# Performance work log

Measured on AMD Instinct MI355X. Metric: run time of the kernel, lower is better.

Reference implementation:

```python
import jax, jax.numpy as jnp
import numpy as np

DELTA_VAR = 0.5
DELTA_DIST = 1.5
ALPHA, BETA, GAMMA = 1.0, 1.0, 0.001
EPS = 1e-8


def _safe_sqrt(x):
    # sqrt with zero (sub)gradient at 0, matching torch.norm's subgradient
    pos = x > 0
    return jnp.sqrt(jnp.where(pos, x, 1.0)) * pos


def setup_inputs() -> dict:
    key = jax.random.key(0)
    k1, k2, k3 = jax.random.split(key, 3)
    B, F, H, W, K = 8, 16, 384, 384, 24
    x = jax.random.normal(k1, (B, F, H, W), dtype=jnp.float32)
    n_clusters = jax.random.randint(k2, (B,), 2, K + 1).astype(jnp.int32)
    # per-pixel instance labels, in-range per sample
    labels = jax.random.randint(k3, (B, H * W), 0, K) % n_clusters[:, None]
    target = jax.nn.one_hot(labels, K, dtype=jnp.float32)  # (B, L, K)
    target = target.transpose(0, 2, 1).reshape(B, K, H, W)
    return {"input": x, "target": target, "n_clusters": n_clusters}


def reference(input, target, n_clusters):
    B, F, H, W = input.shape
    K = target.shape[1]
    x = input.reshape(B, F, H * W)          # (b, f, l)
    t = target.reshape(B, K, H * W)         # (b, c, l)
    nc = n_clusters.astype(x.dtype)         # (b,)
    valid = (jnp.arange(K)[None, :] < n_clusters[:, None]).astype(x.dtype)  # (b, c)

    # ---- cluster means (masked segment mean; padded clusters -> 0) ----
    t_sum = t.sum(-1)                                        # (b, c)
    sums = jnp.einsum('bfl,bcl->bfc', x, t)                  # (b, f, c)
    means = sums / (t_sum[:, None, :] + EPS) * valid[:, None, :]

    # ---- variance term: ||x_l - mu_c||_2 via quadratic expansion ----
    x2 = jnp.sum(x * x, axis=1)                              # (b, l)
    m2 = jnp.sum(means * means, axis=1)                      # (b, c)
    xm = jnp.einsum('bfl,bfc->bcl', x, means)                # (b, c, l)
    d2 = jnp.maximum(x2[:, None, :] - 2.0 * xm + m2[:, :, None], 0.0)
    dist = _safe_sqrt(d2)                                    # (b, c, l)
    var = jnp.maximum(dist - DELTA_VAR, 0.0) ** 2 * t        # (b, c, l)
    c_var = var.sum(-1) / (t_sum + EPS)                      # (b, c)
    var_per = (c_var * valid).sum(-1) / (nc + EPS)
    var_term = jnp.sum(var_per * (nc > 0)) / B

    # ---- distance term: hinge on pairwise mean distances ----
    mm = jnp.einsum('bfc,bfd->bcd', means, means)            # (b, c, c)
    pd2 = jnp.maximum(m2[:, :, None] - 2.0 * mm + m2[:, None, :], 0.0)
    pdist = _safe_sqrt(pd2)                                  # (b, c, c)
    offdiag = 1.0 - jnp.eye(K, dtype=x.dtype)
    pair_mask = valid[:, :, None] * valid[:, None, :] * offdiag
    hinge = jnp.maximum(2.0 * DELTA_DIST - pdist, 0.0) ** 2 * pair_mask
    dist_per = hinge.sum((1, 2)) / (2.0 * nc * (nc - 1.0) + EPS)
    dist_term = jnp.sum(dist_per * (nc > 1)) / B

    # ---- regularization term: mean over valid clusters of ||mu_c|| ----
    norms = _safe_sqrt(m2)                                   # (b, c)
    reg_term = jnp.sum((norms * valid).sum(-1) / nc) / B

    return ALPHA * var_term + BETA * dist_term + GAMMA * reg_term
```

## Files before the change

### kernel.cpp

```cpp
#include <hip/hip_runtime.h>

#define B 8
#define F 16
#define K 24
#define L 147456
#define NSEG (L / 256)
#define NBLKB 288
#define KB_ITER 4
#define EPSF 1e-8f
#define DELTA_VAR 0.5f
#define DELTA_DIST 1.5f
#define GAMMA 0.001f

typedef float fx4 __attribute__((ext_vector_type(4)));
typedef short bf16x8 __attribute__((ext_vector_type(8)));
typedef float f32x4 __attribute__((ext_vector_type(4)));

#define OFF_CNTP 3538944
#define OFF_VARP 3981312
#define OFF_CNT  4423680
#define OFF_VSUM 4424448
#define OFF_MEAN 4425216
#define OFF_LAB  4437504

__device__ __forceinline__ short to_bf16(float v) {
    unsigned u = __float_as_uint(v);
    return (short)((u + 0x7FFFu + ((u >> 16) & 1u)) >> 16);
}

__global__ __launch_bounds__(256) void ka_labels(const float* __restrict__ t,
                                                 unsigned char* __restrict__ labels,
                                                 float* __restrict__ cnt_part) {
    const int blk = blockIdx.x;
    const int b = blk / NSEG;
    const int seg = blk % NSEG;
    const int tid = threadIdx.x;
    const int l = seg * 256 + tid;

    int lab = 0;
    #pragma unroll
    for (int c = 0; c < K; ++c) {
        float tv = __builtin_nontemporal_load(&t[(size_t)(b * K + c) * L + l]);
        lab += c * (tv > 0.5f);
    }
    labels[(size_t)b * L + l] = (unsigned char)lab;

    __shared__ float cnt[32];
    if (tid < 32) cnt[tid] = 0.f;
    __syncthreads();
    atomicAdd(&cnt[lab], 1.f);
    __syncthreads();
    if (tid < K) cnt_part[blk * K + tid] = cnt[tid];
}

__global__ __launch_bounds__(256) void kr_reduce24(const float* __restrict__ part,
                                                   float* __restrict__ out) {
    const int bc = blockIdx.x;
    const int b = bc / K;
    const int c = bc % K;
    const int tid = threadIdx.x;
    float s = 0.f;
    for (int j = tid; j < NSEG; j += 256) s += part[(b * NSEG + j) * K + c];
    __shared__ float red[256];
    red[tid] = s;
    __syncthreads();
    for (int st = 128; st > 0; st >>= 1) {
        if (tid < st) red[tid] += red[tid + st];
        __syncthreads();
    }
    if (tid == 0) out[bc] = red[0];
}

__global__ __launch_bounds__(256) void kb_mfma(const float* __restrict__ x,
                                               const unsigned char* __restrict__ labels,
                                               float* __restrict__ sum_part) {
    const int gblk = blockIdx.x;
    const int b = gblk / NBLKB;
    const int blk = gblk % NBLKB;
    const int tid = threadIdx.x;
    const int wave = tid >> 6;
    const int lane = tid & 63;
    const int n = lane & 15;
    const int q = lane >> 4;
    const int wid = blk * 4 + wave;

    f32x4 acc0 = {0.f, 0.f, 0.f, 0.f};
    f32x4 acc1 = {0.f, 0.f, 0.f, 0.f};
    const float* xr_base = x + (size_t)(b * F + n) * L + q * 8;
    const unsigned char* lb_base = labels + (size_t)b * L + q * 8;

    #pragma unroll
    for (int it = 0; it < KB_ITER; ++it) {
        const int px0 = (wid * KB_ITER + it) * 32;
        fx4 xa = *(const fx4*)(xr_base + px0);
        fx4 xc = *(const fx4*)(xr_base + px0 + 4);
        const unsigned* lp = (const unsigned*)(lb_base + px0);
        unsigned l0 = lp[0], l1 = lp[1];

        bf16x8 afrag;
        afrag[0] = to_bf16(xa.x); afrag[1] = to_bf16(xa.y);
        afrag[2] = to_bf16(xa.z); afrag[3] = to_bf16(xa.w);
        afrag[4] = to_bf16(xc.x); afrag[5] = to_bf16(xc.y);
        afrag[6] = to_bf16(xc.z); afrag[7] = to_bf16(xc.w);

        bf16x8 bf0, bf1;
        #pragma unroll
        for (int j = 0; j < 8; ++j) {
            int lj = (j < 4) ? ((l0 >> (8 * j)) & 0xFF) : ((l1 >> (8 * (j - 4))) & 0xFF);
            bf0[j] = (lj == n)      ? (short)0x3F80 : (short)0;
            bf1[j] = (lj == n + 16) ? (short)0x3F80 : (short)0;
        }
        acc0 = __builtin_amdgcn_mfma_f32_16x16x32_bf16(afrag, bf0, acc0, 0, 0, 0);
        acc1 = __builtin_amdgcn_mfma_f32_16x16x32_bf16(afrag, bf1, acc1, 0, 0, 0);
    }

    __shared__ float sacc[4][F * K];
    #pragma unroll
    for (int r = 0; r < 4; ++r) {
        int f = q * 4 + r;
        sacc[wave][f * K + n] = acc0[r];
        if (n < 8) sacc[wave][f * K + 16 + n] = acc1[r];
    }
    __syncthreads();
    for (int i = tid; i < F * K; i += 256) {
        float v = sacc[0][i] + sacc[1][i] + sacc[2][i] + sacc[3][i];
        sum_part[(size_t)gblk * (F * K) + i] = v;
    }
}

__global__ __launch_bounds__(256) void k2_means(const float* __restrict__ sum_part,
                                                const float* __restrict__ counts,
                                                const int* __restrict__ ncl,
                                                float* __restrict__ means) {
    const int idx = blockIdx.x * 256 + threadIdx.x;
    if (idx >= B * F * K) return;
    const int b = idx / (F * K);
    const int r = idx % (F * K);
    const int c = r % K;

    float s = 0.f;
    const float* base = sum_part + (size_t)b * NBLKB * (F * K) + r;
    #pragma unroll 4
    for (int j = 0; j < NBLKB; ++j) s += base[(size_t)j * (F * K)];

    float valid = (c < ncl[b]) ? 1.f : 0.f;
    means[idx] = s / (counts[b * K + c] + EPSF) * valid;
}

__global__ __launch_bounds__(256, 2) void kc_var(const float* __restrict__ x,
                                                 const unsigned char* __restrict__ labels,
                                                 const float* __restrict__ means,
                                                 float* __restrict__ var_part) {
    const int blk = blockIdx.x;
    const int b = blk / NSEG;
    const int seg = blk % NSEG;
    const int tid = threadIdx.x;
    const int w = tid >> 6;

    __shared__ float m[F * K];
    __shared__ float vacc[4][32];

    const int l = seg * 256 + tid;
    const int lab = labels[(size_t)b * L + l];

    float xv[F];
    #pragma unroll
    for (int f = 0; f < F; ++f) xv[f] = x[(size_t)(b * F + f) * L + l];

    for (int i = tid; i < F * K; i += 256) m[i] = means[b * F * K + i];
    if ((tid & 63) < 32) vacc[w][tid & 63] = 0.f;
    __syncthreads();

    float d2 = 0.f;
    #pragma unroll
    for (int f = 0; f < F; ++f) {
        float u = xv[f] - m[f * K + lab];
        d2 += u * u;
    }
    float s = fmaxf(sqrtf(d2) - DELTA_VAR, 0.f);
    s *= s;
    atomicAdd(&vacc[w][lab], s);

    __syncthreads();
    if (tid < K) {
        float v = vacc[0][tid] + vacc[1][tid] + vacc[2][tid] + vacc[3][tid];
        var_part[blk * K + tid] = v;
    }
}

__global__ __launch_bounds__(256) void k4_final(const float* __restrict__ means,
                                                const float* __restrict__ counts,
                                                const float* __restrict__ varsums,
                                                const int* __restrict__ ncl,
                                                float* __restrict__ out) {
    __shared__ float red[256];
    const int tid = threadIdx.x;
    float total = 0.f;
    for (int idx = tid; idx < B * K * K; idx += 256) {
        int b = idx / (K * K);
        int r = idx % (K * K);
        int c = r / K;
        int d = r % K;
        int ncb = ncl[b];
        float fnc = (float)ncb;
        if (d == 0 && c < ncb && ncb > 0) {
            float cv = varsums[b * K + c] / (counts[b * K + c] + EPSF);
            total += cv / (fnc + EPSF) * (1.0f / B);
            float m2 = 0.f;
            #pragma unroll
            for (int f = 0; f < F; ++f) {
                float mv = means[(b * F + f) * K + c];
                m2 += mv * mv;
            }
            total += GAMMA * sqrtf(m2) / fnc * (1.0f / B);
        }
        if (c != d && c < ncb && d < ncb && ncb > 1) {
            float pd2 = 0.f;
            #pragma unroll
            for (int f = 0; f < F; ++f) {
                float diff = means[(b * F + f) * K + c] - means[(b * F + f) * K + d];
                pd2 += diff * diff;
            }
            float h = fmaxf(2.f * DELTA_DIST - sqrtf(pd2), 0.f);
            total += h * h / (2.f * fnc * (fnc - 1.f) + EPSF) * (1.0f / B);
        }
    }
    red[tid] = total;
    __syncthreads();
    for (int s = 128; s > 0; s >>= 1) {
        if (tid < s) red[tid] += red[tid + s];
        __syncthreads();
    }
    if (tid == 0) out[0] = red[0];
}

extern "C" void kernel_launch(void* const* d_in, const int* in_sizes, int n_in,
                              void* d_out, int out_size, void* d_ws, size_t ws_size,
                              hipStream_t stream) {
    const float* x = (const float*)d_in[0];
    const float* t = (const float*)d_in[1];
    const int* ncl = (const int*)d_in[2];
    float* out = (float*)d_out;

    char* ws = (char*)d_ws;
    float* sum_part = (float*)ws;
    float* cnt_part = (float*)(ws + OFF_CNTP);
    float* var_part = (float*)(ws + OFF_VARP);
    float* counts   = (float*)(ws + OFF_CNT);
    float* varsums  = (float*)(ws + OFF_VSUM);
    float* means    = (float*)(ws + OFF_MEAN);
    unsigned char* labels = (unsigned char*)(ws + OFF_LAB);

    ka_labels <<<B * NSEG, 256, 0, stream>>>(t, labels, cnt_part);
    kr_reduce24<<<B * K, 256, 0, stream>>>(cnt_part, counts);
    kb_mfma   <<<B * NBLKB, 256, 0, stream>>>(x, labels, sum_part);
    k2_means  <<<(B * F * K + 255) / 256, 256, 0, stream>>>(sum_part, counts, ncl, means);
    kc_var    <<<B * NSEG, 256, 0, stream>>>(x, labels, means, var_part);
    kr_reduce24<<<B * K, 256, 0, stream>>>(var_part, varsums);
    k4_final  <<<1, 256, 0, stream>>>(means, counts, varsums, ncl, out);
}
```

Measured before the change: 259.9 us.

## Fuse label extraction and cluster-sum MFMA into one kernel, merge count reduction into means

Label extraction, per-chunk histograms and the bf16 MFMA segment sums now run in a single kernel, with labels staged in shared memory instead of being re-read from global. The count reduction is folded into the means kernel, which runs one block per batch, and partial buffers are transposed so reductions read contiguously. This removes two launches and an intermediate global pass, at the cost of a low-parallelism means reduction over 8 blocks.

```diff
diff --git a/kernel.cpp b/kernel.cpp
--- a/kernel.cpp
+++ b/kernel.cpp
@@ -4,9 +4,9 @@
 #define F 16
 #define K 24
 #define L 147456
+#define CHUNK1 1024
+#define NCH1 (L / CHUNK1)
 #define NSEG (L / 256)
-#define NBLKB 288
-#define KB_ITER 4
 #define EPSF 1e-8f
 #define DELTA_VAR 0.5f
 #define DELTA_DIST 1.5f
@@ -16,86 +16,75 @@
 typedef short bf16x8 __attribute__((ext_vector_type(8)));
 typedef float f32x4 __attribute__((ext_vector_type(4)));
 
-#define OFF_CNTP 3538944
-#define OFF_VARP 3981312
-#define OFF_CNT  4423680
-#define OFF_VSUM 4424448
-#define OFF_MEAN 4425216
-#define OFF_LAB  4437504
+#define OFF_CNTP 1769472
+#define OFF_VARP 1880064
+#define OFF_CNT  2322432
+#define OFF_VSUM 2323200
+#define OFF_MEAN 2323968
+#define OFF_LAB  2336256
 
 __device__ __forceinline__ short to_bf16(float v) {
     unsigned u = __float_as_uint(v);
     return (short)((u + 0x7FFFu + ((u >> 16) & 1u)) >> 16);
 }
 
-__global__ __launch_bounds__(256) void ka_labels(const float* __restrict__ t,
-                                                 unsigned char* __restrict__ labels,
-                                                 float* __restrict__ cnt_part) {
-    const int blk = blockIdx.x;
-    const int b = blk / NSEG;
-    const int seg = blk % NSEG;
-    const int tid = threadIdx.x;
-    const int l = seg * 256 + tid;
-
-    int lab = 0;
-    #pragma unroll
-    for (int c = 0; c < K; ++c) {
-        float tv = __builtin_nontemporal_load(&t[(size_t)(b * K + c) * L + l]);
-        lab += c * (tv > 0.5f);
-    }
-    labels[(size_t)b * L + l] = (unsigned char)lab;
-
-    __shared__ float cnt[32];
-    if (tid < 32) cnt[tid] = 0.f;
-    __syncthreads();
-    atomicAdd(&cnt[lab], 1.f);
-    __syncthreads();
-    if (tid < K) cnt_part[blk * K + tid] = cnt[tid];
-}
-
-__global__ __launch_bounds__(256) void kr_reduce24(const float* __restrict__ part,
-                                                   float* __restrict__ out) {
-    const int bc = blockIdx.x;
-    const int b = bc / K;
-    const int c = bc % K;
-    const int tid = threadIdx.x;
-    float s = 0.f;
-    for (int j = tid; j < NSEG; j += 256) s += part[(b * NSEG + j) * K + c];
-    __shared__ float red[256];
-    red[tid] = s;
-    __syncthreads();
-    for (int st = 128; st > 0; st >>= 1) {
-        if (tid < st) red[tid] += red[tid + st];
-        __syncthreads();
-    }
-    if (tid == 0) out[bc] = red[0];
-}
-
-__global__ __launch_bounds__(256) void kb_mfma(const float* __restrict__ x,
-                                               const unsigned char* __restrict__ labels,
-                                               float* __restrict__ sum_part) {
+__global__ __launch_bounds__(256) void k1_fused(const float* __restrict__ t,
+                                                const float* __restrict__ x,
+                                                unsigned char* __restrict__ labels,
+                                                float* __restrict__ cnt_part,
+                                                float* __restrict__ sum_part) {
     const int gblk = blockIdx.x;
-    const int b = gblk / NBLKB;
-    const int blk = gblk % NBLKB;
+    const int b = gblk / NCH1;
+    const int ch = gblk % NCH1;
     const int tid = threadIdx.x;
     const int wave = tid >> 6;
     const int lane = tid & 63;
+
+    __shared__ unsigned char slab[CHUNK1];
+    __shared__ float hist[4][32];
+    __shared__ float sacc[4][F * K];
+
+    if (lane < 32) hist[wave][lane] = 0.f;
+
+    const int px = ch * CHUNK1 + tid * 4;
+    const fx4* t4 = (const fx4*)t;
+    int lab0 = 0, lab1 = 0, lab2 = 0, lab3 = 0;
+    #pragma unroll
+    for (int c = 0; c < K; ++c) {
+        fx4 tv = __builtin_nontemporal_load(&t4[((size_t)(b * K + c) * L + px) >> 2]);
+        lab0 += c * (tv.x > 0.5f);
+        lab1 += c * (tv.y > 0.5f);
+        lab2 += c * (tv.z > 0.5f);
+        lab3 += c * (tv.w > 0.5f);
+    }
+    uchar4 lv = make_uchar4((unsigned char)lab0, (unsigned char)lab1,
+                            (unsigned char)lab2, (unsigned char)lab3);
+    *(uchar4*)&labels[(size_t)b * L + px] = lv;
+    *(uchar4*)&slab[tid * 4] = lv;
+    atomicAdd(&hist[wave][lab0], 1.f);
+    atomicAdd(&hist[wave][lab1], 1.f);
+    atomicAdd(&hist[wave][lab2], 1.f);
+    atomicAdd(&hist[wave][lab3], 1.f);
+    __syncthreads();
+
+    if (tid < K) {
+        float v = hist[0][tid] + hist[1][tid] + hist[2][tid] + hist[3][tid];
+        cnt_part[tid * (B * NCH1) + gblk] = v;
+    }
+
     const int n = lane & 15;
     const int q = lane >> 4;
-    const int wid = blk * 4 + wave;
-
     f32x4 acc0 = {0.f, 0.f, 0.f, 0.f};
     f32x4 acc1 = {0.f, 0.f, 0.f, 0.f};
-    const float* xr_base = x + (size_t)(b * F + n) * L + q * 8;
-    const unsigned char* lb_base = labels + (size_t)b * L + q * 8;
-
-    #pragma unroll
-    for (int it = 0; it < KB_ITER; ++it) {
-        const int px0 = (wid * KB_ITER + it) * 32;
-        fx4 xa = *(const fx4*)(xr_base + px0);
-        fx4 xc = *(const fx4*)(xr_base + px0 + 4);
-        const unsigned* lp = (const unsigned*)(lb_base + px0);
-        unsigned l0 = lp[0], l1 = lp[1];
+    const float* xr = x + (size_t)(b * F + n) * L + ch * CHUNK1 + wave * 256 + q * 8;
+    const unsigned char* sl = slab + wave * 256 + q * 8;
+
+    #pragma unroll 2
+    for (int it = 0; it < 8; ++it) {
+        fx4 xa = *(const fx4*)(xr + it * 32);
+        fx4 xc = *(const fx4*)(xr + it * 32 + 4);
+        unsigned l0 = *(const unsigned*)(sl + it * 32);
+        unsigned l1 = *(const unsigned*)(sl + it * 32 + 4);
 
         bf16x8 afrag;
         afrag[0] = to_bf16(xa.x); afrag[1] = to_bf16(xa.y);
@@ -114,7 +103,6 @@
         acc1 = __builtin_amdgcn_mfma_f32_16x16x32_bf16(afrag, bf1, acc1, 0, 0, 0);
     }
 
-    __shared__ float sacc[4][F * K];
     #pragma unroll
     for (int r = 0; r < 4; ++r) {
         int f = q * 4 + r;
@@ -128,23 +116,44 @@
     }
 }
 
-__global__ __launch_bounds__(256) void k2_means(const float* __restrict__ sum_part,
-                                                const float* __restrict__ counts,
+__global__ __launch_bounds__(256) void k2_means(const float* __restrict__ cnt_part,
+                                                const float* __restrict__ sum_part,
                                                 const int* __restrict__ ncl,
+                                                float* __restrict__ counts,
                                                 float* __restrict__ means) {
-    const int idx = blockIdx.x * 256 + threadIdx.x;
-    if (idx >= B * F * K) return;
-    const int b = idx / (F * K);
-    const int r = idx % (F * K);
-    const int c = r % K;
-
-    float s = 0.f;
-    const float* base = sum_part + (size_t)b * NBLKB * (F * K) + r;
-    #pragma unroll 4
-    for (int j = 0; j < NBLKB; ++j) s += base[(size_t)j * (F * K)];
-
-    float valid = (c < ncl[b]) ? 1.f : 0.f;
-    means[idx] = s / (counts[b * K + c] + EPSF) * valid;
+    const int b = blockIdx.x;
+    const int tid = threadIdx.x;
+    __shared__ float cl[8][K];
+    __shared__ float cs[K];
+
+    if (tid < 192) {
+        int c = tid >> 3, grp = tid & 7;
+        const float* row = cnt_part + c * (B * NCH1) + b * NCH1 + grp * 18;
+        float s = 0.f;
+        #pragma unroll
+        for (int j = 0; j < 18; ++j) s += row[j];
+        cl[grp][c] = s;
+    }
+    __syncthreads();
+    if (tid < K) {
+        float s = 0.f;
+        #pragma unroll
+        for (int g = 0; g < 8; ++g) s += cl[g][tid];
+        cs[tid] = s;
+        counts[b * K + tid] = s;
+    }
+    __syncthreads();
+
+    const int ncb = ncl[b];
+    for (int r = tid; r < F * K; r += 256) {
+        float s = 0.f;
+        const float* base = sum_part + (size_t)b * NCH1 * (F * K) + r;
+        #pragma unroll 4
+        for (int j = 0; j < NCH1; ++j) s += base[(size_t)j * (F * K)];
+        int c = r % K;
+        float valid = (c < ncb) ? 1.f : 0.f;
+        means[b * F * K + r] = s / (cs[c] + EPSF) * valid;
+    }
 }
 
 __global__ __launch_bounds__(256, 2) void kc_var(const float* __restrict__ x,
@@ -184,8 +193,27 @@
     __syncthreads();
     if (tid < K) {
         float v = vacc[0][tid] + vacc[1][tid] + vacc[2][tid] + vacc[3][tid];
-        var_part[blk * K + tid] = v;
-    }
+        var_part[tid * (B * NSEG) + blk] = v;
+    }
+}
+
+__global__ __launch_bounds__(256) void kr_reduce(const float* __restrict__ part,
+                                                 float* __restrict__ out) {
+    const int bc = blockIdx.x;
+    const int b = bc / K;
+    const int c = bc % K;
+    const int tid = threadIdx.x;
+    const float* row = part + c * (B * NSEG) + b * NSEG;
+    float s = 0.f;
+    for (int j = tid; j < NSEG; j += 256) s += row[j];
+    __shared__ float red[256];
+    red[tid] = s;
+    __syncthreads();
+    for (int st = 128; st > 0; st >>= 1) {
+        if (tid < st) red[tid] += red[tid + st];
+        __syncthreads();
+    }
+    if (tid == 0) out[bc] = red[0];
 }
 
 __global__ __launch_bounds__(256) void k4_final(const float* __restrict__ means,
@@ -251,11 +279,9 @@
     float* means    = (float*)(ws + OFF_MEAN);
     unsigned char* labels = (unsigned char*)(ws + OFF_LAB);
 
-    ka_labels <<<B * NSEG, 256, 0, stream>>>(t, labels, cnt_part);
-    kr_reduce24<<<B * K, 256, 0, stream>>>(cnt_part, counts);
-    kb_mfma   <<<B * NBLKB, 256, 0, stream>>>(x, labels, sum_part);
-    k2_means  <<<(B * F * K + 255) / 256, 256, 0, stream>>>(sum_part, counts, ncl, means);
-    kc_var    <<<B * NSEG, 256, 0, stream>>>(x, labels, means, var_part);
-    kr_reduce24<<<B * K, 256, 0, stream>>>(var_part, varsums);
-    k4_final  <<<1, 256, 0, stream>>>(means, counts, varsums, ncl, out);
-}
+    k1_fused <<<B * NCH1, 256, 0, stream>>>(t, x, labels, cnt_part, sum_part);
+    k2_means <<<B, 256, 0, stream>>>(cnt_part, sum_part, ncl, counts, means);
+    kc_var   <<<B * NSEG, 256, 0, stream>>>(x, labels, means, var_part);
+    kr_reduce<<<B * K, 256, 0, stream>>>(var_part, varsums);
+    k4_final <<<1, 256, 0, stream>>>(means, counts, varsums, ncl, out);
+}
```

Measured after the change: 257.4 us. About the same (-1.0%).
